# Kernel tuning notes

Measured on AMD Instinct MI355X. Metric: run time of the kernel, lower is better.

Reference implementation:

```python
import jax, jax.numpy as jnp
import numpy as np

VOCAB = 50000
EMB = 300      # embedding_dim
VDIM = 16      # value_dim
QDIM = 200     # query_dim
NHEAD = 16     # head_num
HIDDEN = VDIM * NHEAD  # 256


def setup_inputs() -> dict:
    key = jax.random.key(0)
    ks = jax.random.split(key, 9)
    news_batch = jax.random.randint(ks[0], (32, 50, 20), 0, VOCAB)  # [B, his, L]
    emb_table = jax.random.normal(ks[1], (VOCAB, EMB), dtype=jnp.float32)
    queryWeight = jax.random.normal(ks[2], (NHEAD, EMB, EMB), dtype=jnp.float32) * 0.05
    queryBias = jax.random.normal(ks[3], (NHEAD, 1, EMB), dtype=jnp.float32) * 0.05
    valueWeight = jax.random.normal(ks[4], (NHEAD, EMB, VDIM), dtype=jnp.float32) * 0.05
    valueBias = jax.random.normal(ks[5], (NHEAD, 1, VDIM), dtype=jnp.float32) * 0.05
    keyW = jax.random.normal(ks[6], (QDIM, HIDDEN), dtype=jnp.float32) * 0.05  # nn.Linear weight [out,in]
    keyB = jax.random.normal(ks[7], (QDIM,), dtype=jnp.float32) * 0.05
    query = jax.random.normal(ks[8], (1, QDIM), dtype=jnp.float32)
    return {"news_batch": news_batch, "emb_table": emb_table,
            "queryWeight": queryWeight, "queryBias": queryBias,
            "valueWeight": valueWeight, "valueBias": valueBias,
            "keyW": keyW, "keyB": keyB, "query": query}


def reference(news_batch, emb_table, queryWeight, queryBias, valueWeight, valueBias, keyW, keyB, query):
    # Dropout in eval mode -> identity.
    x = emb_table[news_batch]                                   # [B,S,L,E]
    B, S, L, E = x.shape
    # per-head query projection: mha_key.matmul(queryWeight) + queryBias
    q = jnp.einsum('bsle,nef->bsnlf', x, queryWeight) + queryBias  # [B,S,N,L,E]
    # ScaledDpAttention(q, key=x, value=x), scale by sqrt(query last dim) = sqrt(E)
    scores = jnp.einsum('bsnlf,bsmf->bsnlm', q, x) / jnp.sqrt(jnp.float32(E))
    attn = jax.nn.softmax(scores, axis=-1)
    ctx = jnp.einsum('bsnlm,bsme->bsnle', attn, x)               # [B,S,N,L,E]
    v = jnp.einsum('bsnle,nev->bsnlv', ctx, valueWeight) + valueBias  # [B,S,N,L,V]
    # transpose(-2,-3) then merge heads -> [B,S,L,N*V]
    mha_embedding = jnp.swapaxes(v, -2, -3).reshape(B, S, L, HIDDEN)
    # additive attention pooling
    add_key = jnp.tanh(mha_embedding @ keyW.T + keyB)            # [B,S,L,QDIM]
    s2 = jnp.einsum('qd,bsld->bsql', query, add_key) / jnp.sqrt(jnp.float32(QDIM))
    a2 = jax.nn.softmax(s2, axis=-1)                             # [B,S,1,L]
    news_repr = jnp.einsum('bsql,bslh->bsqh', a2, mha_embedding)[:, :, 0, :]  # [B,S,H]
    news_embedding = mha_embedding.reshape(B, S, L, 1, HIDDEN)   # level=1
    return news_embedding, news_repr
```

## Files before the change

kernel.cpp:

```cpp
#include <hip/hip_runtime.h>
#include <math.h>

#define NBS 1600
#define LL 20
#define EE 300
#define NH 16
#define VD 16
#define HID 256
#define QD 200

typedef short bf16x8 __attribute__((ext_vector_type(8)));
typedef float f32x4 __attribute__((ext_vector_type(4)));

__device__ __forceinline__ short f2b(float f) {
    union { float f; unsigned u; } c; c.f = f;
    unsigned r = (c.u + 0x7FFFu + ((c.u >> 16) & 1u)) >> 16;
    return (short)r;
}

__device__ __forceinline__ float b2f(short s) {
    union { unsigned u; float f; } c; c.u = ((unsigned)(unsigned short)s) << 16;
    return c.f;
}

__device__ __forceinline__ float ftanh(float a) {
    a = fminf(fmaxf(a, -15.f), 15.f);
    float t = __expf(2.f * a);
    return (t - 1.f) / (t + 1.f);
}

__device__ __forceinline__ void gload16(const short* g, short* l) {
    __builtin_amdgcn_global_load_lds(
        (const __attribute__((address_space(1))) unsigned int*)g,
        (__attribute__((address_space(3))) unsigned int*)l, 16, 0, 0);
}


__global__ void build_all(const int* __restrict__ news, const float* __restrict__ emb,
                          const float* __restrict__ vW, const float* __restrict__ vB,
                          const float* __restrict__ keyW,
                          short* __restrict__ Xb, short* __restrict__ WvT,
                          short* __restrict__ kwb) {
    int idx = blockIdx.x * 256 + threadIdx.x;
    if (idx < 2560000) {
        int i = idx / 80, e4 = (idx % 80) * 4;
        short4 o;
        if (e4 < 300) {
            const float4 v = *reinterpret_cast<const float4*>(emb + (size_t)news[i] * EE + e4);
            o.x = f2b(v.x); o.y = f2b(v.y); o.z = f2b(v.z); o.w = f2b(v.w);
        } else if (e4 == 300) {
            o.x = (short)0x3F80; o.y = 0; o.z = 0; o.w = 0;
        } else {
            o.x = o.y = o.z = o.w = 0;
        }
        *reinterpret_cast<short4*>(Xb + (size_t)i * 320 + e4) = o;
        return;
    }
    idx -= 2560000;
    if (idx < 81920) {
        int c = idx / 320, e = idx % 320;
        int n = c >> 4, vd = c & 15;
        float val = (e < EE) ? vW[((size_t)n * EE + e) * VD + vd]
                             : (e == EE ? vB[n * VD + vd] : 0.f);
        WvT[idx] = f2b(val);
        return;
    }
    idx -= 81920;
    if (idx < 65536) {
        int d = idx >> 8;
        kwb[idx] = (d < QD) ? f2b(keyW[idx]) : (short)0;
    }
}

__global__ __launch_bounds__(1024) void build_wqt_lin(
    const float* __restrict__ qW, const float* __restrict__ qB, short* __restrict__ WqT)
{
    __shared__ float t[32][33];
    const int n = blockIdx.z;
    const int e0 = blockIdx.x * 32, f0 = blockIdx.y * 32;
    const int tx = threadIdx.x, ty = threadIdx.y;
    const int e = e0 + ty, f = f0 + tx;
    t[ty][tx] = (e < EE && f < EE) ? qW[((size_t)n * EE + e) * EE + f] : 0.f;
    __syncthreads();
    const int fo = f0 + ty, eo = e0 + tx;
    float val;
    if (fo >= EE)      val = 0.f;
    else if (eo < EE)  val = t[tx][ty];
    else if (eo == EE) val = qB[n * EE + fo];
    else               val = 0.f;
    WqT[((size_t)n * 320 + fo) * 320 + eo] = f2b(val);
}

__global__ __launch_bounds__(256) void gemm_xv(
    const short* __restrict__ Xb, const short* __restrict__ WvT, short* __restrict__ xv)
{
    const int nt0 = blockIdx.x * 128;
    const size_t mt0 = (size_t)blockIdx.y * 128;
    const int tid = threadIdx.x, wave = tid >> 6, lane = tid & 63;
    const int lr = lane & 15, lg = lane >> 4;
    const int wm = wave & 1, wn = wave >> 1;

    __shared__ short As[128][68];
    __shared__ short Bs[128][68];
    f32x4 acc[4][4] = {};

    for (int ks = 0; ks < 5; ++ks) {
        __syncthreads();
        for (int u = 0; u < 4; ++u) {
            int idx = u * 256 + tid;
            int rr = idx >> 3, c8 = idx & 7;
            *reinterpret_cast<bf16x8*>(&As[rr][c8 * 8]) =
                *reinterpret_cast<const bf16x8*>(Xb + (mt0 + rr) * 320 + ks * 64 + c8 * 8);
            *reinterpret_cast<bf16x8*>(&Bs[rr][c8 * 8]) =
                *reinterpret_cast<const bf16x8*>(WvT + (size_t)(nt0 + rr) * 320 + ks * 64 + c8 * 8);
        }
        __syncthreads();
        #pragma unroll
        for (int kk = 0; kk < 2; ++kk) {
            bf16x8 af[4], bfv[4];
            #pragma unroll
            for (int f = 0; f < 4; ++f)
                af[f] = *reinterpret_cast<const bf16x8*>(&As[wm * 64 + f * 16 + lr][kk * 32 + lg * 8]);
            #pragma unroll
            for (int f = 0; f < 4; ++f)
                bfv[f] = *reinterpret_cast<const bf16x8*>(&Bs[wn * 64 + f * 16 + lr][kk * 32 + lg * 8]);
            #pragma unroll
            for (int i = 0; i < 4; ++i)
                #pragma unroll
                for (int j = 0; j < 4; ++j)
                    acc[i][j] = __builtin_amdgcn_mfma_f32_16x16x32_bf16(af[i], bfv[j], acc[i][j], 0, 0, 0);
        }
    }
    #pragma unroll
    for (int i = 0; i < 4; ++i)
        #pragma unroll
        for (int j = 0; j < 4; ++j)
            #pragma unroll
            for (int r = 0; r < 4; ++r)
                xv[(mt0 + wm * 64 + i * 16 + lg * 4 + r) * 256 + nt0 + wn * 64 + j * 16 + lr]
                    = f2b(acc[i][j][r]);
}

__global__ __launch_bounds__(256, 2) void qsv(
    const short* __restrict__ Xb,
    const short* __restrict__ WqT,
    const short* __restrict__ xv,
    float*       __restrict__ out1,
    short*       __restrict__ mhb)
{
    const int g = blockIdx.x;
    const int n = blockIdx.y;
    const int tid = threadIdx.x, wave = tid >> 6, lane = tid & 63;
    const int lr = lane & 15, lg = lane >> 4;
    const size_t row0 = (size_t)g * 80;

    __shared__ short lds[25920];

    const short* gp[13];
    #pragma unroll
    for (int k = 0; k < 13; ++k) {
        const int s = k * 256 + tid;
        if (s < 640) {
            const int row = s >> 3, p = s & 7;
            gp[k] = Xb + (row0 + row) * 320 + (p ^ (row & 7)) * 8;
        } else if (s < 3200) {
            const int s2 = s - 640;
            const int row = s2 >> 3, p = s2 & 7;
            gp[k] = WqT + (size_t)(n * 320 + row) * 320 + (p ^ (row & 7)) * 8;
        } else {
            gp[k] = Xb;
        }
    }

    const int b = wave;
    bf16x8 bv;
    #pragma unroll
    for (int j = 0; j < 8; ++j) {
        int m = lg * 8 + j; if (m > 19) m = 19;
        bv[j] = xv[(row0 + b * 20 + m) * 256 + n * 16 + lr];
    }

    const int sw = (lr & 7);

    f32x4 acc[5][5] = {};
    for (int ks = 0; ks < 5; ++ks) {
        __syncthreads();
        const int ko = ks * 64;
        #pragma unroll
        for (int k = 0; k < 12; ++k)
            gload16(gp[k] + ko, lds + (size_t)(k * 256 + tid) * 8);
        if (tid < 128)
            gload16(gp[12] + ko, lds + (size_t)(3072 + tid) * 8);
        __syncthreads();
        #pragma unroll
        for (int sub = 0; sub < 2; ++sub) {
            bf16x8 af[5], bfr[5];
            #pragma unroll
            for (int i = 0; i < 5; ++i)
                af[i] = *reinterpret_cast<const bf16x8*>(
                    lds + (i * 16 + lr) * 64 + ((sub * 4 + lg) ^ sw) * 8);
            #pragma unroll
            for (int j = 0; j < 5; ++j)
                bfr[j] = *reinterpret_cast<const bf16x8*>(
                    lds + 5120 + (wave * 80 + j * 16 + lr) * 64 + ((sub * 4 + lg) ^ sw) * 8);
            #pragma unroll
            for (int i = 0; i < 5; ++i)
                #pragma unroll
                for (int j = 0; j < 5; ++j)
                    acc[i][j] = __builtin_amdgcn_mfma_f32_16x16x32_bf16(af[i], bfr[j], acc[i][j], 0, 0, 0);
        }
    }
    __syncthreads();

    #pragma unroll
    for (int i = 0; i < 5; ++i)
        #pragma unroll
        for (int j = 0; j < 5; ++j)
            #pragma unroll
            for (int r = 0; r < 4; ++r)
                lds[(i * 16 + lg * 4 + r) * 324 + wave * 80 + j * 16 + lr] = f2b(acc[i][j][r]);

    const int rA0 = b * 20 + lr;
    int rA1 = b * 20 + 16 + lr; if (rA1 > 79) rA1 = 79;
    bf16x8 xpre0[10], xpre1[10];
    #pragma unroll
    for (int ks = 0; ks < 10; ++ks) {
        xpre0[ks] = *reinterpret_cast<const bf16x8*>(Xb + (row0 + rA0) * 320 + ks * 32 + lg * 8);
        xpre1[ks] = *reinterpret_cast<const bf16x8*>(Xb + (row0 + rA1) * 320 + ks * 32 + lg * 8);
    }
    __syncthreads();

    float w0[2][4], w1[2][4];
    {
        f32x4 s[2][2] = {};
        #pragma unroll
        for (int ks = 0; ks < 10; ++ks) {
            const int kc = ks * 32 + lg * 8;
            bf16x8 a0 = *reinterpret_cast<const bf16x8*>(lds + rA0 * 324 + kc);
            bf16x8 a1 = *reinterpret_cast<const bf16x8*>(lds + rA1 * 324 + kc);
            s[0][0] = __builtin_amdgcn_mfma_f32_16x16x32_bf16(a0, xpre0[ks], s[0][0], 0, 0, 0);
            s[0][1] = __builtin_amdgcn_mfma_f32_16x16x32_bf16(a0, xpre1[ks], s[0][1], 0, 0, 0);
            s[1][0] = __builtin_amdgcn_mfma_f32_16x16x32_bf16(a1, xpre0[ks], s[1][0], 0, 0, 0);
            s[1][1] = __builtin_amdgcn_mfma_f32_16x16x32_bf16(a1, xpre1[ks], s[1][1], 0, 0, 0);
        }

        const float scl = 0.057735026918962584f;
        #pragma unroll
        for (int mts = 0; mts < 2; ++mts) {
            #pragma unroll
            for (int r = 0; r < 4; ++r) {
                float v0 = s[mts][0][r] * scl;
                float v1 = s[mts][1][r] * scl;
                float mx = (lr < 4) ? fmaxf(v0, v1) : v0;
                mx = fmaxf(mx, __shfl_xor(mx, 1));
                mx = fmaxf(mx, __shfl_xor(mx, 2));
                mx = fmaxf(mx, __shfl_xor(mx, 4));
                mx = fmaxf(mx, __shfl_xor(mx, 8));
                float e0 = __expf(v0 - mx);
                float e1 = (lr < 4) ? __expf(v1 - mx) : 0.f;
                float sm = e0 + e1;
                sm += __shfl_xor(sm, 1);
                sm += __shfl_xor(sm, 2);
                sm += __shfl_xor(sm, 4);
                sm += __shfl_xor(sm, 8);
                const float inv = 1.f / sm;
                w0[mts][r] = e0 * inv;
                w1[mts][r] = e1 * inv;
            }
        }
    }

    short* atw = lds + b * 6480;
    {
        int* az = reinterpret_cast<int*>(atw);
        #pragma unroll
        for (int i = 0; i < 9; ++i) {
            const int ix = lane + i * 64;
            if (ix < 544) az[ix] = 0;
        }
    }
    #pragma unroll
    for (int mts = 0; mts < 2; ++mts)
        #pragma unroll
        for (int r = 0; r < 4; ++r) {
            const int row = mts * 16 + lg * 4 + r;
            if (row < LL) {
                atw[row * 34 + lr]      = f2b(w0[mts][r]);
                atw[row * 34 + 16 + lr] = f2b(w1[mts][r]);
            }
        }

    bf16x8 va0 = *reinterpret_cast<const bf16x8*>(atw + lr * 34 + lg * 8);
    bf16x8 va1 = *reinterpret_cast<const bf16x8*>(atw + (16 + lr) * 34 + lg * 8);
    f32x4 z = {0.f, 0.f, 0.f, 0.f};
    f32x4 v0 = __builtin_amdgcn_mfma_f32_16x16x32_bf16(va0, bv, z, 0, 0, 0);
    f32x4 v1 = __builtin_amdgcn_mfma_f32_16x16x32_bf16(va1, bv, z, 0, 0, 0);
    #pragma unroll
    for (int r = 0; r < 4; ++r) {
        const int rowl = lg * 4 + r;
        const size_t o0 = (row0 + b * 20 + rowl) * 256 + n * 16 + lr;
        out1[o0] = v0[r];
        mhb[o0] = f2b(v0[r]);
        const int rowl1 = 16 + lg * 4 + r;
        if (rowl1 < LL) {
            const size_t o1 = (row0 + b * 20 + rowl1) * 256 + n * 16 + lr;
            out1[o1] = v1[r];
            mhb[o1] = f2b(v1[r]);
        }
    }
}

__global__ __launch_bounds__(256, 4) void gemm_ak2(
    const short* __restrict__ mhb,
    const short* __restrict__ kwb,
    const float* __restrict__ keyB,
    const float* __restrict__ query,
    float*       __restrict__ s2p)
{
    const int nt0 = blockIdx.x * 128;
    const int mt0 = blockIdx.y * 128;
    const int tid = threadIdx.x, wave = tid >> 6, lane = tid & 63;
    const int lr = lane & 15, lg = lane >> 4;
    const int wm = wave & 1, wn = wave >> 1;

    __shared__ short sAB[8192];
    __shared__ float part[128][2];

    const int rA = tid >> 2, c = tid & 3;
    const short* aS0 = mhb + (size_t)(mt0 + rA) * 256 + c * 8;
    const short* aS1 = aS0 + (size_t)64 * 256;
    const short* bS0 = kwb + (size_t)(nt0 + rA) * 256 + c * 8;
    const short* bS1 = bS0 + (size_t)64 * 256;
    short* d0 = sAB + tid * 8;
    short* d1 = sAB + (tid + 256) * 8;
    short* d2 = sAB + (tid + 512) * 8;
    short* d3 = sAB + (tid + 768) * 8;

    f32x4 acc[4][4] = {};
    for (int ks = 0; ks < 8; ++ks) {
        __syncthreads();
        const int ko = ks * 32;
        gload16(aS0 + ko, d0);
        gload16(aS1 + ko, d1);
        gload16(bS0 + ko, d2);
        gload16(bS1 + ko, d3);
        __syncthreads();
        bf16x8 af[4], bfr[4];
        #pragma unroll
        for (int i = 0; i < 4; ++i)
            af[i] = *reinterpret_cast<const bf16x8*>(sAB + (wm * 64 + i * 16 + lr) * 32 + lg * 8);
        #pragma unroll
        for (int j = 0; j < 4; ++j)
            bfr[j] = *reinterpret_cast<const bf16x8*>(sAB + 4096 + (wn * 64 + j * 16 + lr) * 32 + lg * 8);
        #pragma unroll
        for (int i = 0; i < 4; ++i)
            #pragma unroll
            for (int j = 0; j < 4; ++j)
                acc[i][j] = __builtin_amdgcn_mfma_f32_16x16x32_bf16(af[i], bfr[j], acc[i][j], 0, 0, 0);
    }

    #pragma unroll
    for (int i = 0; i < 4; ++i)
        #pragma unroll
        for (int r = 0; r < 4; ++r) {
            float vsum = 0.f;
            #pragma unroll
            for (int j = 0; j < 4; ++j) {
                const int d = nt0 + wn * 64 + j * 16 + lr;
                if (d < QD)
                    vsum = fmaf(query[d], ftanh(acc[i][j][r] + keyB[d]), vsum);
            }
            vsum += __shfl_xor(vsum, 1);
            vsum += __shfl_xor(vsum, 2);
            vsum += __shfl_xor(vsum, 4);
            vsum += __shfl_xor(vsum, 8);
            if (lr == 0)
                part[wm * 64 + i * 16 + lg * 4 + r][wn] = vsum;
        }
    __syncthreads();

    if (tid < 128)
        s2p[(size_t)(mt0 + tid) * 2 + blockIdx.x] = part[tid][0] + part[tid][1];
}

__global__ __launch_bounds__(256) void pool_final(
    const float* __restrict__ s2p,
    const float* __restrict__ out1,
    float*       __restrict__ out2)
{
    const int bs = blockIdx.x;
    const int tid = threadIdx.x;

    __shared__ float s2[LL];

    if (tid < LL) {
        const size_t row = (size_t)bs * 20 + tid;
        s2[tid] = (s2p[row * 2] + s2p[row * 2 + 1]) * 0.07071067811865475f;
    }
    __syncthreads();

    if (tid == 0) {
        float mx = -1e30f;
        #pragma unroll
        for (int l = 0; l < LL; ++l) mx = fmaxf(mx, s2[l]);
        float e[LL], sum = 0.f;
        #pragma unroll
        for (int l = 0; l < LL; ++l) { e[l] = __expf(s2[l] - mx); sum += e[l]; }
        const float inv = 1.f / sum;
        #pragma unroll
        for (int l = 0; l < LL; ++l) s2[l] = e[l] * inv;
    }
    __syncthreads();

    float o = 0.f;
    #pragma unroll
    for (int l = 0; l < LL; ++l)
        o = fmaf(s2[l], out1[((size_t)bs * 20 + l) * 256 + tid], o);
    out2[(size_t)bs * 256 + tid] = o;
}


#define XP 330
#define TP 42
#define AP 34

__global__ __launch_bounds__(1024) void transpose_qw(
    const float* __restrict__ qW, short* __restrict__ wqt)
{
    __shared__ float t[32][33];
    const int n = blockIdx.z;
    const int e0 = blockIdx.x * 32, f0 = blockIdx.y * 32;
    const int tx = threadIdx.x, ty = threadIdx.y;
    const int e = e0 + ty, f = f0 + tx;
    t[ty][tx] = (e < EE && f < EE) ? qW[(size_t)n * EE * EE + e * EE + f] : 0.f;
    __syncthreads();
    const int fo = f0 + ty, eo = e0 + tx;
    if (fo < 304)
        wqt[(size_t)n * 304 * 320 + fo * 320 + eo] = f2b(t[tx][ty]);
}

__global__ void conv_vw(const float* __restrict__ vW, short* __restrict__ wvt) {
    int idx = blockIdx.x * 256 + threadIdx.x;
    if (idx >= NH * VD * 320) return;
    int e = idx % 320;
    int v = (idx / 320) % VD;
    int n = idx / (320 * VD);
    wvt[idx] = (e < EE) ? f2b(vW[(size_t)n * EE * VD + e * VD + v]) : (short)0;
}

__global__ void conv_kw_fb(const float* __restrict__ keyW, short* __restrict__ kwb) {
    int idx = blockIdx.x * 256 + threadIdx.x;
    if (idx >= 256 * 256) return;
    int d = idx >> 8;
    kwb[idx] = (d < QD) ? f2b(keyW[idx]) : (short)0;
}

__global__ __launch_bounds__(512) void nrms_attn_mfma(
    const int*   __restrict__ news,
    const float* __restrict__ emb,
    const short* __restrict__ wqt,
    const float* __restrict__ qB,
    const short* __restrict__ wvt,
    const float* __restrict__ vB,
    float*       __restrict__ out1)
{
    const int bs   = blockIdx.x;
    const int tid  = threadIdx.x;
    const int wave = tid >> 6;
    const int lane = tid & 63;
    const int lr   = lane & 15;
    const int lg   = lane >> 4;

    __shared__ short xs[32][XP];
    __shared__ short xT[320][TP];
    __shared__ short qs[32][XP];
    __shared__ float sc[32][33];
    __shared__ short at[32][AP];

    {
        int* z = (int*)&xs[0][0];
        for (int i = tid; i < 32 * XP / 2; i += 512) z[i] = 0;
        z = (int*)&qs[0][0];
        for (int i = tid; i < 32 * XP / 2; i += 512) z[i] = 0;
        z = (int*)&xT[0][0];
        for (int i = tid; i < 320 * TP / 2; i += 512) z[i] = 0;
    }
    __syncthreads();

    for (int idx = tid; idx < LL * 75; idx += 512) {
        const int l = idx / 75, e4 = (idx % 75) * 4;
        const int row = news[bs * LL + l];
        const float4 v = *reinterpret_cast<const float4*>(emb + (size_t)row * EE + e4);
        const short b0 = f2b(v.x), b1 = f2b(v.y), b2 = f2b(v.z), b3 = f2b(v.w);
        xs[l][e4] = b0; xs[l][e4 + 1] = b1; xs[l][e4 + 2] = b2; xs[l][e4 + 3] = b3;
        xT[e4][l] = b0; xT[e4 + 1][l] = b1; xT[e4 + 2][l] = b2; xT[e4 + 3][l] = b3;
    }
    __syncthreads();

    for (int n = 0; n < NH; ++n) {
        const short* wq = wqt + (size_t)n * 304 * 320;

        for (int p = wave; p < 19; p += 8) {
            f32x4 acc0 = {0.f, 0.f, 0.f, 0.f};
            f32x4 acc1 = {0.f, 0.f, 0.f, 0.f};
            const short* a0p = &xs[lr][lg * 8];
            const short* a1p = &xs[16 + lr][lg * 8];
            const short* bp  = wq + (p * 16 + lr) * 320 + lg * 8;
            #pragma unroll
            for (int k = 0; k < 10; ++k) {
                bf16x8 b  = *reinterpret_cast<const bf16x8*>(bp + k * 32);
                bf16x8 a0 = *reinterpret_cast<const bf16x8*>(a0p + k * 32);
                bf16x8 a1 = *reinterpret_cast<const bf16x8*>(a1p + k * 32);
                acc0 = __builtin_amdgcn_mfma_f32_16x16x32_bf16(a0, b, acc0, 0, 0, 0);
                acc1 = __builtin_amdgcn_mfma_f32_16x16x32_bf16(a1, b, acc1, 0, 0, 0);
            }
            const int col = p * 16 + lr;
            const float bias = (col < EE) ? qB[n * EE + col] : 0.f;
            #pragma unroll
            for (int r = 0; r < 4; ++r) {
                qs[lg * 4 + r][col]      = f2b(acc0[r] + bias);
                qs[16 + lg * 4 + r][col] = f2b(acc1[r] + bias);
            }
        }
        __syncthreads();

        if (wave < 4) {
            const int mt = wave & 1, nt = wave >> 1;
            f32x4 acc = {0.f, 0.f, 0.f, 0.f};
            const short* ap = &qs[mt * 16 + lr][lg * 8];
            const short* bp = &xs[nt * 16 + lr][lg * 8];
            #pragma unroll
            for (int k = 0; k < 10; ++k) {
                bf16x8 a = *reinterpret_cast<const bf16x8*>(ap + k * 32);
                bf16x8 b = *reinterpret_cast<const bf16x8*>(bp + k * 32);
                acc = __builtin_amdgcn_mfma_f32_16x16x32_bf16(a, b, acc, 0, 0, 0);
            }
            #pragma unroll
            for (int r = 0; r < 4; ++r)
                sc[mt * 16 + lg * 4 + r][nt * 16 + lr] = acc[r] * 0.057735026918962584f;
        }
        __syncthreads();

        if (tid < LL) {
            float mx = -1e30f;
            #pragma unroll
            for (int m = 0; m < LL; ++m) mx = fmaxf(mx, sc[tid][m]);
            float ev[LL], sum = 0.f;
            #pragma unroll
            for (int m = 0; m < LL; ++m) { ev[m] = __expf(sc[tid][m] - mx); sum += ev[m]; }
            const float inv = 1.f / sum;
            #pragma unroll
            for (int m = 0; m < LL; ++m) at[tid][m] = f2b(ev[m] * inv);
            #pragma unroll
            for (int m = LL; m < 32; ++m) at[tid][m] = 0;
        } else if (tid < 32) {
            int* zr = (int*)&at[tid][0];
            #pragma unroll
            for (int m = 0; m < 16; ++m) zr[m] = 0;
        }
        __syncthreads();

        for (int p = wave; p < 19; p += 8) {
            bf16x8 b  = *reinterpret_cast<const bf16x8*>(&xT[p * 16 + lr][lg * 8]);
            bf16x8 a0 = *reinterpret_cast<const bf16x8*>(&at[lr][lg * 8]);
            bf16x8 a1 = *reinterpret_cast<const bf16x8*>(&at[16 + lr][lg * 8]);
            f32x4 z = {0.f, 0.f, 0.f, 0.f};
            f32x4 c0 = __builtin_amdgcn_mfma_f32_16x16x32_bf16(a0, b, z, 0, 0, 0);
            f32x4 c1 = __builtin_amdgcn_mfma_f32_16x16x32_bf16(a1, b, z, 0, 0, 0);
            const int col = p * 16 + lr;
            #pragma unroll
            for (int r = 0; r < 4; ++r) {
                qs[lg * 4 + r][col]      = f2b(c0[r]);
                qs[16 + lg * 4 + r][col] = f2b(c1[r]);
            }
        }
        __syncthreads();

        if (wave < 2) {
            const int mt = wave;
            f32x4 acc = {0.f, 0.f, 0.f, 0.f};
            const short* ap = &qs[mt * 16 + lr][lg * 8];
            const short* bp = wvt + (size_t)n * VD * 320 + lr * 320 + lg * 8;
            #pragma unroll
            for (int k = 0; k < 10; ++k) {
                bf16x8 a = *reinterpret_cast<const bf16x8*>(ap + k * 32);
                bf16x8 b = *reinterpret_cast<const bf16x8*>(bp + k * 32);
                acc = __builtin_amdgcn_mfma_f32_16x16x32_bf16(a, b, acc, 0, 0, 0);
            }
            #pragma unroll
            for (int r = 0; r < 4; ++r) {
                const int row = mt * 16 + lg * 4 + r;
                if (row < LL)
                    out1[((size_t)bs * LL + row) * HID + n * VD + lr] = acc[r] + vB[n * VD + lr];
            }
        }
        __syncthreads();
    }
}

__global__ __launch_bounds__(256) void nrms_pool_mfma(
    const float* __restrict__ out1,
    const short* __restrict__ kwb,
    const float* __restrict__ keyB,
    const float* __restrict__ query,
    float*       __restrict__ out2)
{
    const int bs   = blockIdx.x;
    const int tid  = threadIdx.x;
    const int wave = tid >> 6;
    const int lane = tid & 63;
    const int lr   = lane & 15;
    const int lg   = lane >> 4;

    __shared__ float mh[LL][257];
    __shared__ short mhbl[32][264];
    __shared__ float s2p[32];

    for (int i = tid; i < 12 * 128; i += 256) {
        const int r = 20 + i / 128, c = (i % 128) * 2;
        *reinterpret_cast<int*>(&mhbl[r][c]) = 0;
    }
    if (tid < 32) s2p[tid] = 0.f;

    for (int idx = tid; idx < LL * 64; idx += 256) {
        const int l = idx >> 6, h4 = (idx & 63) * 4;
        const float4 v = *reinterpret_cast<const float4*>(out1 + ((size_t)bs * LL + l) * HID + h4);
        mh[l][h4] = v.x; mh[l][h4 + 1] = v.y; mh[l][h4 + 2] = v.z; mh[l][h4 + 3] = v.w;
        mhbl[l][h4] = f2b(v.x); mhbl[l][h4 + 1] = f2b(v.y);
        mhbl[l][h4 + 2] = f2b(v.z); mhbl[l][h4 + 3] = f2b(v.w);
    }
    __syncthreads();

    for (int t = wave; t < 26; t += 4) {
        const int mt = t & 1, nt = t >> 1;
        f32x4 acc = {0.f, 0.f, 0.f, 0.f};
        const short* ap = &mhbl[mt * 16 + lr][lg * 8];
        const short* bp = kwb + (nt * 16 + lr) * 256 + lg * 8;
        #pragma unroll
        for (int k = 0; k < 8; ++k) {
            bf16x8 a = *reinterpret_cast<const bf16x8*>(ap + k * 32);
            bf16x8 b = *reinterpret_cast<const bf16x8*>(bp + k * 32);
            acc = __builtin_amdgcn_mfma_f32_16x16x32_bf16(a, b, acc, 0, 0, 0);
        }
        const int d = nt * 16 + lr;
        const float qd = (d < QD) ? query[d] : 0.f;
        const float kb = (d < QD) ? keyB[d] : 0.f;
        float vals[4];
        #pragma unroll
        for (int r = 0; r < 4; ++r) vals[r] = qd * ftanh(acc[r] + kb);
        #pragma unroll
        for (int off = 1; off < 16; off <<= 1) {
            #pragma unroll
            for (int r = 0; r < 4; ++r) vals[r] += __shfl_xor(vals[r], off);
        }
        if (lr == 0) {
            #pragma unroll
            for (int r = 0; r < 4; ++r)
                atomicAdd(&s2p[mt * 16 + lg * 4 + r], vals[r]);
        }
    }
    __syncthreads();

    if (tid == 0) {
        float mx = -1e30f;
        #pragma unroll
        for (int l = 0; l < LL; ++l) mx = fmaxf(mx, s2p[l] * 0.07071067811865475f);
        float sum = 0.f;
        float e[LL];
        #pragma unroll
        for (int l = 0; l < LL; ++l) { e[l] = __expf(s2p[l] * 0.07071067811865475f - mx); sum += e[l]; }
        const float inv = 1.f / sum;
        #pragma unroll
        for (int l = 0; l < LL; ++l) s2p[l] = e[l] * inv;
    }
    __syncthreads();

    {
        const int h = tid;
        float acc = 0.f;
        #pragma unroll
        for (int l = 0; l < LL; ++l) acc = fmaf(s2p[l], mh[l][h], acc);
        out2[(size_t)bs * HID + h] = acc;
    }
}


extern "C" void kernel_launch(void* const* d_in, const int* in_sizes, int n_in,
                              void* d_out, int out_size, void* d_ws, size_t ws_size,
                              hipStream_t stream) {
    const int*   news  = (const int*)d_in[0];
    const float* emb   = (const float*)d_in[1];
    const float* qW    = (const float*)d_in[2];
    const float* qB    = (const float*)d_in[3];
    const float* vW    = (const float*)d_in[4];
    const float* vB    = (const float*)d_in[5];
    const float* keyW  = (const float*)d_in[6];
    const float* keyB  = (const float*)d_in[7];
    const float* query = (const float*)d_in[8];

    float* out1 = (float*)d_out;
    float* out2 = out1 + 8192000;

    const size_t BASE_SH = 10240000ull + 1638400 + 81920 + 8192000
                         + 65536 + 8192000 + 128000;
    const size_t BASE_B  = BASE_SH * 2;

    if (ws_size >= BASE_B) {
        short* Xb   = (short*)d_ws;
        short* WqT  = Xb + 10240000;
        short* WvT  = WqT + 1638400;
        short* xv   = WvT + 81920;
        short* kwb2 = xv + 8192000;
        short* mhb  = kwb2 + 65536;
        float* s2p  = (float*)(mhb + 8192000);

        hipLaunchKernelGGL(build_all, dim3(10577), dim3(256), 0, stream,
                           news, emb, vW, vB, keyW, Xb, WvT, kwb2);
        hipLaunchKernelGGL(build_wqt_lin, dim3(10, 10, 16), dim3(32, 32), 0, stream, qW, qB, WqT);
        hipLaunchKernelGGL(gemm_xv, dim3(2, 250), dim3(256), 0, stream, Xb, WvT, xv);
        hipLaunchKernelGGL(qsv, dim3(400, 16), dim3(256), 0, stream,
                           Xb, WqT, xv, out1, mhb);
        hipLaunchKernelGGL(gemm_ak2, dim3(2, 250), dim3(256), 0, stream,
                           mhb, kwb2, keyB, query, s2p);
        hipLaunchKernelGGL(pool_final, dim3(NBS), dim3(256), 0, stream, s2p, out1, out2);
    } else {
        short* wqt  = (short*)d_ws;
        short* wvt  = wqt + (size_t)NH * 304 * 320;
        short* kwb2 = wvt + (size_t)NH * VD * 320;

        hipLaunchKernelGGL(transpose_qw, dim3(10, 10, 16), dim3(32, 32), 0, stream, qW, wqt);
        hipLaunchKernelGGL(conv_vw, dim3(320), dim3(256), 0, stream, vW, wvt);
        hipLaunchKernelGGL(conv_kw_fb, dim3(256), dim3(256), 0, stream, keyW, kwb2);
        hipLaunchKernelGGL(nrms_attn_mfma, dim3(NBS), dim3(512), 0, stream,
                           news, emb, wqt, qB, wvt, vB, out1);
        hipLaunchKernelGGL(nrms_pool_mfma, dim3(NBS), dim3(256), 0, stream,
                           out1, kwb2, keyB, query, out2);
    }
}
```

Measured before the change: 249.3 us.

## Double-buffer qsv K-loop staging to overlap global loads with MFMA

Splits the qsv kernel's K loop into 32-wide stages held in two LDS buffers, so the global-to-LDS loads for the next stage are issued while MFMAs run on the current one. The XOR swizzle is retuned for 32-element rows. This targets the load-wait stalls between the two barriers in each old iteration. It doubles the number of barriers and leaves fewer loads per stage, which could cut into the overlap gained.

```diff
diff --git a/kernel.cpp b/kernel.cpp
--- a/kernel.cpp
+++ b/kernel.cpp
@@ -141,6 +141,34 @@
                     = f2b(acc[i][j][r]);
 }
 
+#define QSV_STAGE(BUF, KS)                                                     \
+    {                                                                          \
+        const int ko_ = (KS) * 32;                                             \
+        _Pragma("unroll")                                                      \
+        for (int k = 0; k < 6; ++k)                                            \
+            gload16(gp[k] + ko_, (BUF) + (size_t)(k * 256 + tid) * 8);         \
+        if (tid < 64)                                                          \
+            gload16(gp[6] + ko_, (BUF) + (size_t)(1536 + tid) * 8);            \
+    }
+
+#define QSV_COMPUTE(BUF)                                                       \
+    {                                                                          \
+        bf16x8 af[5], bfr[5];                                                  \
+        _Pragma("unroll")                                                      \
+        for (int i = 0; i < 5; ++i)                                            \
+            af[i] = *reinterpret_cast<const bf16x8*>(                          \
+                (BUF) + (i * 16 + lr) * 32 + (lg ^ (lr & 3)) * 8);             \
+        _Pragma("unroll")                                                      \
+        for (int j = 0; j < 5; ++j)                                            \
+            bfr[j] = *reinterpret_cast<const bf16x8*>(                         \
+                (BUF) + 2560 + (wave * 80 + j * 16 + lr) * 32 + (lg ^ (lr & 3)) * 8); \
+        _Pragma("unroll")                                                      \
+        for (int i = 0; i < 5; ++i)                                            \
+            _Pragma("unroll")                                                  \
+            for (int j = 0; j < 5; ++j)                                        \
+                acc[i][j] = __builtin_amdgcn_mfma_f32_16x16x32_bf16(af[i], bfr[j], acc[i][j], 0, 0, 0); \
+    }
+
 __global__ __launch_bounds__(256, 2) void qsv(
     const short* __restrict__ Xb,
     const short* __restrict__ WqT,
@@ -155,18 +183,20 @@
     const size_t row0 = (size_t)g * 80;
 
     __shared__ short lds[25920];
-
-    const short* gp[13];
-    #pragma unroll
-    for (int k = 0; k < 13; ++k) {
+    short* bufA = lds;
+    short* bufB = lds + 12800;
+
+    const short* gp[7];
+    #pragma unroll
+    for (int k = 0; k < 7; ++k) {
         const int s = k * 256 + tid;
-        if (s < 640) {
-            const int row = s >> 3, p = s & 7;
-            gp[k] = Xb + (row0 + row) * 320 + (p ^ (row & 7)) * 8;
-        } else if (s < 3200) {
-            const int s2 = s - 640;
-            const int row = s2 >> 3, p = s2 & 7;
-            gp[k] = WqT + (size_t)(n * 320 + row) * 320 + (p ^ (row & 7)) * 8;
+        if (s < 320) {
+            const int row = s >> 2, p = s & 3;
+            gp[k] = Xb + (row0 + row) * 320 + (p ^ (row & 3)) * 8;
+        } else if (s < 1600) {
+            const int s2 = s - 320;
+            const int row = s2 >> 2, p = s2 & 3;
+            gp[k] = WqT + (size_t)(n * 320 + row) * 320 + (p ^ (row & 3)) * 8;
         } else {
             gp[k] = Xb;
         }
@@ -180,37 +210,18 @@
         bv[j] = xv[(row0 + b * 20 + m) * 256 + n * 16 + lr];
     }
 
-    const int sw = (lr & 7);
-
     f32x4 acc[5][5] = {};
-    for (int ks = 0; ks < 5; ++ks) {
-        __syncthreads();
-        const int ko = ks * 64;
-        #pragma unroll
-        for (int k = 0; k < 12; ++k)
-            gload16(gp[k] + ko, lds + (size_t)(k * 256 + tid) * 8);
-        if (tid < 128)
-            gload16(gp[12] + ko, lds + (size_t)(3072 + tid) * 8);
-        __syncthreads();
-        #pragma unroll
-        for (int sub = 0; sub < 2; ++sub) {
-            bf16x8 af[5], bfr[5];
-            #pragma unroll
-            for (int i = 0; i < 5; ++i)
-                af[i] = *reinterpret_cast<const bf16x8*>(
-                    lds + (i * 16 + lr) * 64 + ((sub * 4 + lg) ^ sw) * 8);
-            #pragma unroll
-            for (int j = 0; j < 5; ++j)
-                bfr[j] = *reinterpret_cast<const bf16x8*>(
-                    lds + 5120 + (wave * 80 + j * 16 + lr) * 64 + ((sub * 4 + lg) ^ sw) * 8);
-            #pragma unroll
-            for (int i = 0; i < 5; ++i)
-                #pragma unroll
-                for (int j = 0; j < 5; ++j)
-                    acc[i][j] = __builtin_amdgcn_mfma_f32_16x16x32_bf16(af[i], bfr[j], acc[i][j], 0, 0, 0);
-        }
-    }
-    __syncthreads();
+    QSV_STAGE(bufA, 0);
+    __syncthreads();
+    #pragma unroll
+    for (int kp = 0; kp < 5; ++kp) {
+        if (kp * 2 + 1 < 10) QSV_STAGE(bufB, kp * 2 + 1);
+        QSV_COMPUTE(bufA);
+        __syncthreads();
+        if (kp * 2 + 2 < 10) QSV_STAGE(bufA, kp * 2 + 2);
+        QSV_COMPUTE(bufB);
+        __syncthreads();
+    }
 
     #pragma unroll
     for (int i = 0; i < 5; ++i)
```

Result: slower. 260.3 us (+4.4%).
